# Optimization experiments

Measured on AMD Instinct MI355X. Metric: run time of the kernel, lower is better.

Reference implementation:

```python
import jax, jax.numpy as jnp
import numpy as np

SOS = 1  # start-of-sequence token id (module references a global SOS)
VOCAB, EMBED, HIDDEN = 32000, 512, 1024

def setup_inputs() -> dict:
    key = jax.random.key(0)
    ks = jax.random.split(key, 8)
    B = 32
    s = lambda k, shape, scale: jax.random.normal(k, shape, dtype=jnp.float32) * scale
    return {
        "init_hidden": s(ks[0], (1, B, HIDDEN), 1.0),
        "encoder_outputs": s(ks[1], (B, 64, HIDDEN), 1.0),
        "tgt_len": 64,
        "embedding": s(ks[2], (VOCAB, EMBED), 1.0),
        "w_ih": s(ks[3], (3 * HIDDEN, EMBED), 0.03),
        "b_ih": s(ks[4], (3 * HIDDEN,), 0.03),
        "w_hh": s(ks[5], (3 * HIDDEN, HIDDEN), 0.03),
        "b_hh": s(ks[6], (3 * HIDDEN,), 0.03),
        "w_out": s(ks[7], (VOCAB, HIDDEN), 0.03),
        "b_out": jnp.zeros((VOCAB,), dtype=jnp.float32),
    }

def reference(init_hidden, encoder_outputs, tgt_len, embedding, w_ih, b_ih, w_hh, b_hh, w_out, b_out):
    B = init_hidden.shape[1]
    h0 = init_hidden[0]                       # [B, H] (num_layers=1)
    tok0 = jnp.full((B,), SOS, dtype=jnp.int32)

    def step(carry, _):
        h, tok = carry
        x = jnp.tanh(embedding[tok])          # [B, E]
        gi = x @ w_ih.T + b_ih                # [B, 3H]
        gh = h @ w_hh.T + b_hh                # [B, 3H]
        i_r, i_z, i_n = jnp.split(gi, 3, axis=-1)
        h_r, h_z, h_n = jnp.split(gh, 3, axis=-1)
        r = jax.nn.sigmoid(i_r + h_r)
        z = jax.nn.sigmoid(i_z + h_z)
        n = jnp.tanh(i_n + r * h_n)
        h_new = (1.0 - z) * n + z * h         # [B, H]
        logp = jax.nn.log_softmax(h_new @ w_out.T + b_out, axis=-1)  # [B, V]
        tok_new = jnp.argmax(logp, axis=-1).astype(jnp.int32)
        return (h_new, tok_new), logp

    (_, _), outputs = jax.lax.scan(step, (h0, tok0), None, length=tgt_len)
    return outputs                            # [T, B, V] log-probs (matches list of squeezed outputs)
```

## Files before the change

### kernel.cpp

```cpp
#include <hip/hip_runtime.h>
#include <math.h>

#define B    32
#define H    1024
#define EMB  512
#define V    32000
#define SOS  1

#define OFF_X   0
#define OFF_HA  16384
#define OFF_HB  49152
#define OFF_P   81920
#define OFF_C   145920
#define OFF_HHI 147968
#define OFF_HLO 164352
#define OFF_WHI 180736
#define OFF_WLO 16564736

#define NEG_INF (-3.0e38f)

typedef float f4v   __attribute__((ext_vector_type(4)));
typedef short short8v __attribute__((ext_vector_type(8)));
typedef float f32x4 __attribute__((ext_vector_type(4)));

#define MF(a,b,c) c = __builtin_amdgcn_mfma_f32_16x16x32_bf16(a, b, c, 0, 0, 0)

__device__ __forceinline__ unsigned short rnb(float x) {
    unsigned u = __float_as_uint(x);
    unsigned r = u + 0x7FFFu + ((u >> 16) & 1u);
    return (unsigned short)(r >> 16);
}
__device__ __forceinline__ float bfh(unsigned short s) {
    return __uint_as_float(((unsigned)s) << 16);
}
__device__ __forceinline__ void sm_merge(float& m, float& l, int& a,
                                         float om, float ol, int oa)
{
    const bool take = (om > m) || (om == m && oa < a);
    const float mn = take ? om : m;
    const int   an = take ? oa : a;
    l = l * expf(m - mn) + ol * expf(om - mn);
    m = mn; a = an;
}

__global__ void k_init(const float* __restrict__ ih, const float* __restrict__ emb,
                       const float* __restrict__ wout, float* __restrict__ ws)
{
    const size_t idx = (size_t)blockIdx.x * blockDim.x + threadIdx.x;
    const size_t stride = (size_t)gridDim.x * blockDim.x;
    for (size_t i = idx; i < EMB * B; i += stride)
        ws[OFF_X + i] = tanhf(emb[(size_t)SOS * EMB + (i >> 5)]);
    for (size_t i = idx; i < H * B; i += stride) {
        int j = (int)(i >> 5), b = (int)(i & 31);
        ws[OFF_HA + j * 32 + b] = ih[(size_t)b * H + j];
    }
    short* Whi = (short*)(ws + OFF_WHI);
    short* Wlo = (short*)(ws + OFF_WLO);
    for (size_t i = idx; i < (size_t)V * H; i += stride) {
        const float x = wout[i];
        const unsigned short hi = rnb(x);
        Whi[i] = (short)hi;
        Wlo[i] = (short)rnb(x - bfh(hi));
    }
}

__global__ __launch_bounds__(1024) void k_gru(
    const float* __restrict__ xG, const float* __restrict__ hold,
    const float* __restrict__ wih, const float* __restrict__ bih,
    const float* __restrict__ whh, const float* __restrict__ bhh,
    float* __restrict__ hnew, short* __restrict__ Hhi, short* __restrict__ Hlo)
{
    const int t   = threadIdx.x;
    const int blk = blockIdx.x;
    __shared__ float sred[4 * 1152];

    const int ks = t >> 7;
    const int pl = t & 127;
    const int p  = blk * 128 + pl;
    const int b  = p & 31;
    const int j  = p >> 5;

    float ar = 0.f, az = 0.f, ain = 0.f, ahn = 0.f;
    const int k0 = ks * 192, k1 = k0 + 192;

    const int xe = (k1 < EMB) ? k1 : EMB;
    for (int k = k0; k < xe; k += 4) {
        const float u0 = xG[(k + 0) * 32 + b];
        const float u1 = xG[(k + 1) * 32 + b];
        const float u2 = xG[(k + 2) * 32 + b];
        const float u3 = xG[(k + 3) * 32 + b];
        const float4 w0 = *(const float4*)&wih[(size_t)(0 * H + j) * EMB + k];
        const float4 w1 = *(const float4*)&wih[(size_t)(1 * H + j) * EMB + k];
        const float4 w2 = *(const float4*)&wih[(size_t)(2 * H + j) * EMB + k];
        ar  = fmaf(w0.x, u0, fmaf(w0.y, u1, fmaf(w0.z, u2, fmaf(w0.w, u3, ar))));
        az  = fmaf(w1.x, u0, fmaf(w1.y, u1, fmaf(w1.z, u2, fmaf(w1.w, u3, az))));
        ain = fmaf(w2.x, u0, fmaf(w2.y, u1, fmaf(w2.z, u2, fmaf(w2.w, u3, ain))));
    }
    const int hs = (k0 > EMB) ? k0 : EMB;
    for (int k = hs; k < k1; k += 4) {
        const int kh = k - EMB;
        const float u0 = hold[(kh + 0) * 32 + b];
        const float u1 = hold[(kh + 1) * 32 + b];
        const float u2 = hold[(kh + 2) * 32 + b];
        const float u3 = hold[(kh + 3) * 32 + b];
        const float4 w0 = *(const float4*)&whh[(size_t)(0 * H + j) * H + kh];
        const float4 w1 = *(const float4*)&whh[(size_t)(1 * H + j) * H + kh];
        const float4 w2 = *(const float4*)&whh[(size_t)(2 * H + j) * H + kh];
        ar  = fmaf(w0.x, u0, fmaf(w0.y, u1, fmaf(w0.z, u2, fmaf(w0.w, u3, ar))));
        az  = fmaf(w1.x, u0, fmaf(w1.y, u1, fmaf(w1.z, u2, fmaf(w1.w, u3, az))));
        ahn = fmaf(w2.x, u0, fmaf(w2.y, u1, fmaf(w2.z, u2, fmaf(w2.w, u3, ahn))));
    }

    sred[0 * 1152 + pl * 9 + ks] = ar;
    sred[1 * 1152 + pl * 9 + ks] = az;
    sred[2 * 1152 + pl * 9 + ks] = ain;
    sred[3 * 1152 + pl * 9 + ks] = ahn;
    __syncthreads();

    if (t < 128) {
        const int pp = blk * 128 + t;
        const int bb = pp & 31, jj = pp >> 5;
        float s0 = 0.f, s1 = 0.f, s2 = 0.f, s3 = 0.f;
#pragma unroll
        for (int q = 0; q < 8; ++q) {
            s0 += sred[0 * 1152 + t * 9 + q];
            s1 += sred[1 * 1152 + t * 9 + q];
            s2 += sred[2 * 1152 + t * 9 + q];
            s3 += sred[3 * 1152 + t * 9 + q];
        }
        float gr  = s0 + bih[jj]         + bhh[jj];
        float gz  = s1 + bih[H + jj]     + bhh[H + jj];
        float gin = s2 + bih[2 * H + jj];
        float ghn = s3 + bhh[2 * H + jj];
        float r = 1.f / (1.f + expf(-gr));
        float z = 1.f / (1.f + expf(-gz));
        float n = tanhf(gin + r * ghn);
        const int hidx = jj * 32 + bb;
        const float hv = (1.f - z) * n + z * hold[hidx];
        hnew[hidx] = hv;
        const unsigned short hi = rnb(hv);
        const unsigned short lo = rnb(hv - bfh(hi));
        const int pidx = (((jj >> 3) * 32) + bb) * 8 + (jj & 7);
        Hhi[pidx] = (short)hi;
        Hlo[pidx] = (short)lo;
    }
}

__global__ __launch_bounds__(512, 4) void k_proj(
    const short* __restrict__ Whi, const short* __restrict__ Wlo,
    const short* __restrict__ Hhi, const short* __restrict__ Hlo,
    const float* __restrict__ bout, float* __restrict__ orow,
    float4* __restrict__ P)
{
    __shared__ float Red[4 * 32 * 33];
    __shared__ float Dt[32 * 68];
    __shared__ float bl[64];
    __shared__ float pm[2][32], pls[2][32];
    __shared__ int   pa[2][32];

    const int t   = threadIdx.x;
    const int blk = blockIdx.x;
    const int r0  = blk * 64;
    const int w   = t >> 6;
    const int mh  = w >> 2;
    const int kq  = w & 3;
    const int l   = t & 63;
    const int lr  = l & 15;
    const int lg  = l >> 4;

    if (t < 64) bl[t] = bout[r0 + t];

    const short* pAh = Whi + (size_t)(r0 + mh * 32 + lr) * H + lg * 8;
    const short* pAl = Wlo + (size_t)(r0 + mh * 32 + lr) * H + lg * 8;
    const short* pBh = Hhi + ((size_t)lg * 32 + lr) * 8;
    const short* pBl = Hlo + ((size_t)lg * 32 + lr) * 8;

    f32x4 acc00 = {0.f, 0.f, 0.f, 0.f};
    f32x4 acc01 = {0.f, 0.f, 0.f, 0.f};
    f32x4 acc10 = {0.f, 0.f, 0.f, 0.f};
    f32x4 acc11 = {0.f, 0.f, 0.f, 0.f};

#pragma unroll 2
    for (int i = 0; i < 8; ++i) {
        const int c = 4 * i + kq;
        const short8v a0h = *(const short8v*)(pAh + c * 32);
        const short8v a0l = *(const short8v*)(pAl + c * 32);
        const short8v a1h = *(const short8v*)(pAh + 16 * H + c * 32);
        const short8v a1l = *(const short8v*)(pAl + 16 * H + c * 32);
        const short8v b0h = *(const short8v*)(pBh + c * 1024);
        const short8v b0l = *(const short8v*)(pBl + c * 1024);
        const short8v b1h = *(const short8v*)(pBh + c * 1024 + 128);
        const short8v b1l = *(const short8v*)(pBl + c * 1024 + 128);
        MF(a0h, b0h, acc00); MF(a0h, b0l, acc00); MF(a0l, b0h, acc00);
        MF(a0h, b1h, acc01); MF(a0h, b1l, acc01); MF(a0l, b1h, acc01);
        MF(a1h, b0h, acc10); MF(a1h, b0l, acc10); MF(a1l, b0h, acc10);
        MF(a1h, b1h, acc11); MF(a1h, b1l, acc11); MF(a1l, b1h, acc11);
    }

    if (kq >= 2) {
        float* rp = Red + (mh * 2 + (kq - 2)) * 1056;
#pragma unroll
        for (int mt = 0; mt < 2; ++mt)
#pragma unroll
            for (int r = 0; r < 4; ++r) {
                const int row = mt * 16 + lg * 4 + r;
                rp[row * 33 + lr]      = mt ? acc10[r] : acc00[r];
                rp[row * 33 + 16 + lr] = mt ? acc11[r] : acc01[r];
            }
    }
    __syncthreads();
    if (kq < 2) {
        const float* rp = Red + (mh * 2 + kq) * 1056;
#pragma unroll
        for (int mt = 0; mt < 2; ++mt)
#pragma unroll
            for (int r = 0; r < 4; ++r) {
                const int row = mt * 16 + lg * 4 + r;
                const float e0 = rp[row * 33 + lr];
                const float e1 = rp[row * 33 + 16 + lr];
                if (mt) { acc10[r] += e0; acc11[r] += e1; }
                else    { acc00[r] += e0; acc01[r] += e1; }
            }
    }
    __syncthreads();
    if (kq == 1) {
        float* rp = Red + mh * 2 * 1056;
#pragma unroll
        for (int mt = 0; mt < 2; ++mt)
#pragma unroll
            for (int r = 0; r < 4; ++r) {
                const int row = mt * 16 + lg * 4 + r;
                rp[row * 33 + lr]      = mt ? acc10[r] : acc00[r];
                rp[row * 33 + 16 + lr] = mt ? acc11[r] : acc01[r];
            }
    }
    __syncthreads();

    if (kq == 0) {
        const float* rp = Red + mh * 2 * 1056;
        float val[2][2][4];
#pragma unroll
        for (int mt = 0; mt < 2; ++mt)
#pragma unroll
            for (int r = 0; r < 4; ++r) {
                const int row = mt * 16 + lg * 4 + r;
                const float bo = bl[mh * 32 + row];
                val[mt][0][r] = (mt ? acc10[r] : acc00[r]) + rp[row * 33 + lr] + bo;
                val[mt][1][r] = (mt ? acc11[r] : acc01[r]) + rp[row * 33 + 16 + lr] + bo;
            }
#pragma unroll
        for (int mt = 0; mt < 2; ++mt)
#pragma unroll
            for (int nt = 0; nt < 2; ++nt)
#pragma unroll
                for (int r = 0; r < 4; ++r)
                    Dt[(nt * 16 + lr) * 68 + mh * 32 + mt * 16 + lg * 4 + r] = val[mt][nt][r];

#pragma unroll
        for (int nt = 0; nt < 2; ++nt) {
            float m = val[0][nt][0], ls = 1.f;
            int a = r0 + mh * 32 + lg * 4;
#pragma unroll
            for (int q = 1; q < 8; ++q) {
                const int mt = q >> 2, r = q & 3;
                const float x = val[mt][nt][r];
                const int row = r0 + mh * 32 + mt * 16 + lg * 4 + r;
                if (x > m) { ls = ls * expf(m - x) + 1.f; m = x; a = row; }
                else       { ls += expf(x - m); }
            }
            sm_merge(m, ls, a, __shfl_xor(m, 16), __shfl_xor(ls, 16), __shfl_xor(a, 16));
            sm_merge(m, ls, a, __shfl_xor(m, 32), __shfl_xor(ls, 32), __shfl_xor(a, 32));
            if (lg == 0) { pm[mh][nt * 16 + lr] = m; pls[mh][nt * 16 + lr] = ls; pa[mh][nt * 16 + lr] = a; }
        }
    }
    __syncthreads();

    if (t < 32) {
        float m = pm[0][t], ls = pls[0][t]; int a = pa[0][t];
        sm_merge(m, ls, a, pm[1][t], pls[1][t], pa[1][t]);
        P[blk * 32 + t] = make_float4(m, ls, (float)a, 0.f);
    }

    const int sb = t >> 4, rq = t & 15;
    const f4v v = *(const f4v*)&Dt[sb * 68 + rq * 4];
    __builtin_nontemporal_store(v, (f4v*)&orow[(size_t)sb * V + r0 + rq * 4]);
}

__global__ __launch_bounds__(256) void k_fin2(
    const float4* __restrict__ partial, const float* __restrict__ emb,
    float* __restrict__ xG, float* __restrict__ C)
{
    const int b = blockIdx.x;
    const int t = threadIdx.x;
    __shared__ float fm[256], fl[256];
    __shared__ int   fa[256], stok;

    float m = NEG_INF, l = 0.f; int a = 0x7FFFFFFF;
    {
        float4 p = partial[t * 32 + b];
        m = p.x; l = p.y; a = (int)p.z;
    }
    if (t + 256 < 500) {
        float4 p = partial[(t + 256) * 32 + b];
        sm_merge(m, l, a, p.x, p.y, (int)p.z);
    }
    fm[t] = m; fl[t] = l; fa[t] = a;
    __syncthreads();
    for (int s = 128; s > 0; s >>= 1) {
        if (t < s) {
            const float om = fm[t + s], ol = fl[t + s];
            const int   oa = fa[t + s];
            float mm = fm[t]; float ll = fl[t]; int aa = fa[t];
            const bool take = (om > mm) || (om == mm && oa < aa);
            const float mn = take ? om : mm;
            const int   an = take ? oa : aa;
            ll = ll * expf(mm - mn) + ol * expf(om - mn);
            fm[t] = mn; fl[t] = ll; fa[t] = an;
        }
        __syncthreads();
    }
    if (t == 0) {
        C[b] = fm[0] + logf(fl[0]);
        stok = fa[0];
    }
    __syncthreads();
    const int TOK = stok;
    for (int k = t; k < EMB; k += 256)
        xG[k * 32 + b] = tanhf(emb[(size_t)TOK * EMB + k]);
}

__global__ __launch_bounds__(256) void k_sub(float* __restrict__ out,
                                             const float* __restrict__ C)
{
    const int r = blockIdx.x;
    const float c = C[r];
    f4v* row = (f4v*)(out + (size_t)r * V);
    for (int v = threadIdx.x; v < V / 4; v += 256) {
        f4v x = __builtin_nontemporal_load(&row[v]);
        x -= c;
        __builtin_nontemporal_store(x, &row[v]);
    }
}

extern "C" void kernel_launch(void* const* d_in, const int* in_sizes, int n_in,
                              void* d_out, int out_size, void* d_ws, size_t ws_size,
                              hipStream_t stream)
{
    const float* p_ih   = (const float*)d_in[0];
    const float* p_emb  = (const float*)d_in[3];
    const float* p_wih  = (const float*)d_in[4];
    const float* p_bih  = (const float*)d_in[5];
    const float* p_whh  = (const float*)d_in[6];
    const float* p_bhh  = (const float*)d_in[7];
    const float* p_wout = (const float*)d_in[8];
    const float* p_bout = (const float*)d_in[9];
    float* out = (float*)d_out;
    float* ws  = (float*)d_ws;
    const int T = out_size / (B * V);

    float*  xG  = ws + OFF_X;
    float*  hA  = ws + OFF_HA;
    float*  hB  = ws + OFF_HB;
    float4* P   = (float4*)(ws + OFF_P);
    float*  C   = ws + OFF_C;
    short*  Hhi = (short*)(ws + OFF_HHI);
    short*  Hlo = (short*)(ws + OFF_HLO);
    short*  Whi = (short*)(ws + OFF_WHI);
    short*  Wlo = (short*)(ws + OFF_WLO);

    k_init<<<2048, 256, 0, stream>>>(p_ih, p_emb, p_wout, ws);

    for (int st = 0; st < T; ++st) {
        float* hold = (st & 1) ? hB : hA;
        float* hnew = (st & 1) ? hA : hB;
        float* orow = out + (size_t)st * B * V;
        k_gru<<<256, 1024, 0, stream>>>(xG, hold, p_wih, p_bih, p_whh, p_bhh,
                                        hnew, Hhi, Hlo);
        k_proj<<<500, 512, 0, stream>>>(Whi, Wlo, Hhi, Hlo, p_bout, orow, P);
        k_fin2<<<B, 256, 0, stream>>>(P, p_emb, xG, C + st * B);
    }
    k_sub<<<T * B, 256, 0, stream>>>(out, C);
}
```

Before: 3.733 ms.

## Interleave GRU weights and switch hidden/input to batch-major layout

```diff
diff --git a/kernel.cpp b/kernel.cpp
--- a/kernel.cpp
+++ b/kernel.cpp
@@ -7,15 +7,16 @@
 #define V    32000
 #define SOS  1
 
-#define OFF_X   0
+#define OFF_XG  0
 #define OFF_HA  16384
 #define OFF_HB  49152
 #define OFF_P   81920
 #define OFF_C   145920
 #define OFF_HHI 147968
 #define OFF_HLO 164352
-#define OFF_WHI 180736
-#define OFF_WLO 16564736
+#define OFF_W3  180736
+#define OFF_WHI 4899328
+#define OFF_WLO 21283328
 
 #define NEG_INF (-3.0e38f)
 
@@ -44,15 +45,38 @@
 }
 
 __global__ void k_init(const float* __restrict__ ih, const float* __restrict__ emb,
-                       const float* __restrict__ wout, float* __restrict__ ws)
+                       const float* __restrict__ wout,
+                       const float* __restrict__ wih, const float* __restrict__ whh,
+                       float* __restrict__ ws)
 {
     const size_t idx = (size_t)blockIdx.x * blockDim.x + threadIdx.x;
     const size_t stride = (size_t)gridDim.x * blockDim.x;
-    for (size_t i = idx; i < EMB * B; i += stride)
-        ws[OFF_X + i] = tanhf(emb[(size_t)SOS * EMB + (i >> 5)]);
+
+    for (size_t i = idx; i < EMB * B; i += stride) {
+        const int k = (int)(i >> 5), b = (int)(i & 31);
+        ws[OFF_XG + b * EMB + k] = tanhf(emb[(size_t)SOS * EMB + k]);
+    }
+    short* Hhi = (short*)(ws + OFF_HHI);
+    short* Hlo = (short*)(ws + OFF_HLO);
     for (size_t i = idx; i < H * B; i += stride) {
-        int j = (int)(i >> 5), b = (int)(i & 31);
-        ws[OFF_HA + j * 32 + b] = ih[(size_t)b * H + j];
+        const int j = (int)(i >> 5), b = (int)(i & 31);
+        const float hv = ih[(size_t)b * H + j];
+        ws[OFF_HA + b * H + j] = hv;
+        const unsigned short hi = rnb(hv);
+        const int pidx = ((j >> 3) * 32 + b) * 8 + (j & 7);
+        Hhi[pidx] = (short)hi;
+        Hlo[pidx] = (short)rnb(hv - bfh(hi));
+    }
+    float* W3 = ws + OFF_W3;
+    for (size_t i = idx; i < (size_t)H * 384 * 12; i += stride) {
+        const int j   = (int)(i / (384 * 12));
+        const int rem = (int)(i % (384 * 12));
+        const int kq  = rem / 12;
+        const int g   = (rem % 12) >> 2;
+        const int e   = rem & 3;
+        const int k   = kq * 4 + e;
+        W3[i] = (k < EMB) ? wih[(size_t)(g * H + j) * EMB + k]
+                          : whh[(size_t)(g * H + j) * H + (k - EMB)];
     }
     short* Whi = (short*)(ws + OFF_WHI);
     short* Wlo = (short*)(ws + OFF_WLO);
@@ -66,8 +90,8 @@
 
 __global__ __launch_bounds__(1024) void k_gru(
     const float* __restrict__ xG, const float* __restrict__ hold,
-    const float* __restrict__ wih, const float* __restrict__ bih,
-    const float* __restrict__ whh, const float* __restrict__ bhh,
+    const float* __restrict__ W3,
+    const float* __restrict__ bih, const float* __restrict__ bhh,
     float* __restrict__ hnew, short* __restrict__ Hhi, short* __restrict__ Hlo)
 {
     const int t   = threadIdx.x;
@@ -84,31 +108,31 @@
     const int k0 = ks * 192, k1 = k0 + 192;
 
     const int xe = (k1 < EMB) ? k1 : EMB;
-    for (int k = k0; k < xe; k += 4) {
-        const float u0 = xG[(k + 0) * 32 + b];
-        const float u1 = xG[(k + 1) * 32 + b];
-        const float u2 = xG[(k + 2) * 32 + b];
-        const float u3 = xG[(k + 3) * 32 + b];
-        const float4 w0 = *(const float4*)&wih[(size_t)(0 * H + j) * EMB + k];
-        const float4 w1 = *(const float4*)&wih[(size_t)(1 * H + j) * EMB + k];
-        const float4 w2 = *(const float4*)&wih[(size_t)(2 * H + j) * EMB + k];
-        ar  = fmaf(w0.x, u0, fmaf(w0.y, u1, fmaf(w0.z, u2, fmaf(w0.w, u3, ar))));
-        az  = fmaf(w1.x, u0, fmaf(w1.y, u1, fmaf(w1.z, u2, fmaf(w1.w, u3, az))));
-        ain = fmaf(w2.x, u0, fmaf(w2.y, u1, fmaf(w2.z, u2, fmaf(w2.w, u3, ain))));
+    {
+        const float* w3 = W3 + ((size_t)j * 384 + (k0 >> 2)) * 12;
+        for (int k = k0; k < xe; k += 4, w3 += 12) {
+            const float4 u  = *(const float4*)&xG[b * EMB + k];
+            const float4 w0 = *(const float4*)&w3[0];
+            const float4 w1 = *(const float4*)&w3[4];
+            const float4 w2 = *(const float4*)&w3[8];
+            ar  = fmaf(w0.x, u.x, fmaf(w0.y, u.y, fmaf(w0.z, u.z, fmaf(w0.w, u.w, ar))));
+            az  = fmaf(w1.x, u.x, fmaf(w1.y, u.y, fmaf(w1.z, u.z, fmaf(w1.w, u.w, az))));
+            ain = fmaf(w2.x, u.x, fmaf(w2.y, u.y, fmaf(w2.z, u.z, fmaf(w2.w, u.w, ain))));
+        }
     }
     const int hs = (k0 > EMB) ? k0 : EMB;
-    for (int k = hs; k < k1; k += 4) {
-        const int kh = k - EMB;
-        const float u0 = hold[(kh + 0) * 32 + b];
-        const float u1 = hold[(kh + 1) * 32 + b];
-        const float u2 = hold[(kh + 2) * 32 + b];
-        const float u3 = hold[(kh + 3) * 32 + b];
-        const float4 w0 = *(const float4*)&whh[(size_t)(0 * H + j) * H + kh];
-        const float4 w1 = *(const float4*)&whh[(size_t)(1 * H + j) * H + kh];
-        const float4 w2 = *(const float4*)&whh[(size_t)(2 * H + j) * H + kh];
-        ar  = fmaf(w0.x, u0, fmaf(w0.y, u1, fmaf(w0.z, u2, fmaf(w0.w, u3, ar))));
-        az  = fmaf(w1.x, u0, fmaf(w1.y, u1, fmaf(w1.z, u2, fmaf(w1.w, u3, az))));
-        ahn = fmaf(w2.x, u0, fmaf(w2.y, u1, fmaf(w2.z, u2, fmaf(w2.w, u3, ahn))));
+    {
+        const float* w3 = W3 + ((size_t)j * 384 + (hs >> 2)) * 12;
+        for (int k = hs; k < k1; k += 4, w3 += 12) {
+            const int kh = k - EMB;
+            const float4 u  = *(const float4*)&hold[b * H + kh];
+            const float4 w0 = *(const float4*)&w3[0];
+            const float4 w1 = *(const float4*)&w3[4];
+            const float4 w2 = *(const float4*)&w3[8];
+            ar  = fmaf(w0.x, u.x, fmaf(w0.y, u.y, fmaf(w0.z, u.z, fmaf(w0.w, u.w, ar))));
+            az  = fmaf(w1.x, u.x, fmaf(w1.y, u.y, fmaf(w1.z, u.z, fmaf(w1.w, u.w, az))));
+            ahn = fmaf(w2.x, u.x, fmaf(w2.y, u.y, fmaf(w2.z, u.z, fmaf(w2.w, u.w, ahn))));
+        }
     }
 
     sred[0 * 1152 + pl * 9 + ks] = ar;
@@ -135,12 +159,12 @@
         float r = 1.f / (1.f + expf(-gr));
         float z = 1.f / (1.f + expf(-gz));
         float n = tanhf(gin + r * ghn);
-        const int hidx = jj * 32 + bb;
-        const float hv = (1.f - z) * n + z * hold[hidx];
-        hnew[hidx] = hv;
+        const float ho = hold[bb * H + jj];
+        const float hv = (1.f - z) * n + z * ho;
+        hnew[bb * H + jj] = hv;
         const unsigned short hi = rnb(hv);
         const unsigned short lo = rnb(hv - bfh(hi));
-        const int pidx = (((jj >> 3) * 32) + bb) * 8 + (jj & 7);
+        const int pidx = ((jj >> 3) * 32 + bb) * 8 + (jj & 7);
         Hhi[pidx] = (short)hi;
         Hlo[pidx] = (short)lo;
     }
@@ -278,7 +302,7 @@
     if (t < 32) {
         float m = pm[0][t], ls = pls[0][t]; int a = pa[0][t];
         sm_merge(m, ls, a, pm[1][t], pls[1][t], pa[1][t]);
-        P[blk * 32 + t] = make_float4(m, ls, (float)a, 0.f);
+        P[(size_t)t * 500 + blk] = make_float4(m, ls, (float)a, 0.f);
     }
 
     const int sb = t >> 4, rq = t & 15;
@@ -287,7 +311,7 @@
 }
 
 __global__ __launch_bounds__(256) void k_fin2(
-    const float4* __restrict__ partial, const float* __restrict__ emb,
+    const float4* __restrict__ P, const float* __restrict__ emb,
     float* __restrict__ xG, float* __restrict__ C)
 {
     const int b = blockIdx.x;
@@ -296,26 +320,21 @@
     __shared__ int   fa[256], stok;
 
     float m = NEG_INF, l = 0.f; int a = 0x7FFFFFFF;
-    {
-        float4 p = partial[t * 32 + b];
+    if (t < 500) {
+        const float4 p = P[(size_t)b * 500 + t];
         m = p.x; l = p.y; a = (int)p.z;
     }
     if (t + 256 < 500) {
-        float4 p = partial[(t + 256) * 32 + b];
+        const float4 p = P[(size_t)b * 500 + t + 256];
         sm_merge(m, l, a, p.x, p.y, (int)p.z);
     }
     fm[t] = m; fl[t] = l; fa[t] = a;
     __syncthreads();
     for (int s = 128; s > 0; s >>= 1) {
         if (t < s) {
-            const float om = fm[t + s], ol = fl[t + s];
-            const int   oa = fa[t + s];
             float mm = fm[t]; float ll = fl[t]; int aa = fa[t];
-            const bool take = (om > mm) || (om == mm && oa < aa);
-            const float mn = take ? om : mm;
-            const int   an = take ? oa : aa;
-            ll = ll * expf(mm - mn) + ol * expf(om - mn);
-            fm[t] = mn; fl[t] = ll; fa[t] = an;
+            sm_merge(mm, ll, aa, fm[t + s], fl[t + s], fa[t + s]);
+            fm[t] = mm; fl[t] = ll; fa[t] = aa;
         }
         __syncthreads();
     }
@@ -326,7 +345,7 @@
     __syncthreads();
     const int TOK = stok;
     for (int k = t; k < EMB; k += 256)
-        xG[k * 32 + b] = tanhf(emb[(size_t)TOK * EMB + k]);
+        xG[b * EMB + k] = tanhf(emb[(size_t)TOK * EMB + k]);
 }
 
 __global__ __launch_bounds__(256) void k_sub(float* __restrict__ out,
@@ -358,23 +377,24 @@
     float* ws  = (float*)d_ws;
     const int T = out_size / (B * V);
 
-    float*  xG  = ws + OFF_X;
+    float*  xG  = ws + OFF_XG;
     float*  hA  = ws + OFF_HA;
     float*  hB  = ws + OFF_HB;
     float4* P   = (float4*)(ws + OFF_P);
     float*  C   = ws + OFF_C;
     short*  Hhi = (short*)(ws + OFF_HHI);
     short*  Hlo = (short*)(ws + OFF_HLO);
+    float*  W3  = ws + OFF_W3;
     short*  Whi = (short*)(ws + OFF_WHI);
     short*  Wlo = (short*)(ws + OFF_WLO);
 
-    k_init<<<2048, 256, 0, stream>>>(p_ih, p_emb, p_wout, ws);
+    k_init<<<2048, 256, 0, stream>>>(p_ih, p_emb, p_wout, p_wih, p_whh, ws);
 
     for (int st = 0; st < T; ++st) {
         float* hold = (st & 1) ? hB : hA;
         float* hnew = (st & 1) ? hA : hB;
         float* orow = out + (size_t)st * B * V;
-        k_gru<<<256, 1024, 0, stream>>>(xG, hold, p_wih, p_bih, p_whh, p_bhh,
+        k_gru<<<256, 1024, 0, stream>>>(xG, hold, W3, p_bih, p_bhh,
                                         hnew, Hhi, Hlo);
         k_proj<<<500, 512, 0, stream>>>(Whi, Wlo, Hhi, Hlo, p_bout, orow, P);
         k_fin2<<<B, 256, 0, stream>>>(P, p_emb, xG, C + st * B);
```

New measurement: 4.734 ms. 26.8% more time.

## Fuse argmax/logsumexp finalize and embedding lookup into GRU kernel

Applied to the files above, without the earlier changes.

```diff
diff --git a/kernel.cpp b/kernel.cpp
--- a/kernel.cpp
+++ b/kernel.cpp
@@ -7,7 +7,6 @@
 #define V    32000
 #define SOS  1
 
-#define OFF_X   0
 #define OFF_HA  16384
 #define OFF_HB  49152
 #define OFF_P   81920
@@ -16,12 +15,14 @@
 #define OFF_HLO 164352
 #define OFF_WHI 180736
 #define OFF_WLO 16564736
+#define OFF_PK  32948736
 
 #define NEG_INF (-3.0e38f)
 
 typedef float f4v   __attribute__((ext_vector_type(4)));
 typedef short short8v __attribute__((ext_vector_type(8)));
 typedef float f32x4 __attribute__((ext_vector_type(4)));
+typedef unsigned long long u64;
 
 #define MF(a,b,c) c = __builtin_amdgcn_mfma_f32_16x16x32_bf16(a, b, c, 0, 0, 0)
 
@@ -42,17 +43,28 @@
     l = l * expf(m - mn) + ol * expf(om - mn);
     m = mn; a = an;
 }
-
-__global__ void k_init(const float* __restrict__ ih, const float* __restrict__ emb,
-                       const float* __restrict__ wout, float* __restrict__ ws)
+__device__ __forceinline__ void sm2(float& m, float& l, float om, float ol)
+{
+    const float mn = fmaxf(m, om);
+    l = l * expf(m - mn) + ol * expf(om - mn);
+    m = mn;
+}
+
+__global__ void k_init(const float* __restrict__ ih, const float* __restrict__ wout,
+                       float* __restrict__ ws)
 {
     const size_t idx = (size_t)blockIdx.x * blockDim.x + threadIdx.x;
     const size_t stride = (size_t)gridDim.x * blockDim.x;
-    for (size_t i = idx; i < EMB * B; i += stride)
-        ws[OFF_X + i] = tanhf(emb[(size_t)SOS * EMB + (i >> 5)]);
+    short* Hhi = (short*)(ws + OFF_HHI);
+    short* Hlo = (short*)(ws + OFF_HLO);
     for (size_t i = idx; i < H * B; i += stride) {
         int j = (int)(i >> 5), b = (int)(i & 31);
-        ws[OFF_HA + j * 32 + b] = ih[(size_t)b * H + j];
+        const float hv = ih[(size_t)b * H + j];
+        ws[OFF_HA + j * 32 + b] = hv;
+        const unsigned short hi = rnb(hv);
+        const int pidx = ((j >> 3) * 32 + b) * 8 + (j & 7);
+        Hhi[pidx] = (short)hi;
+        Hlo[pidx] = (short)rnb(hv - bfh(hi));
     }
     short* Whi = (short*)(ws + OFF_WHI);
     short* Wlo = (short*)(ws + OFF_WLO);
@@ -64,15 +76,78 @@
     }
 }
 
-__global__ __launch_bounds__(1024) void k_gru(
-    const float* __restrict__ xG, const float* __restrict__ hold,
+#define XLF   16896
+#define DSMA  ((XLF + 4608 + 2112 + 32) * 4)
+
+__global__ __launch_bounds__(1024) void k_gruf(
+    const float4* __restrict__ P, const u64* __restrict__ Pkey,
+    const float* __restrict__ emb, const float* __restrict__ hold,
     const float* __restrict__ wih, const float* __restrict__ bih,
     const float* __restrict__ whh, const float* __restrict__ bhh,
-    float* __restrict__ hnew, short* __restrict__ Hhi, short* __restrict__ Hlo)
-{
+    float* __restrict__ hnew, short* __restrict__ Hhi, short* __restrict__ Hlo,
+    float* __restrict__ C_prev, int first)
+{
+    extern __shared__ __align__(16) float dsm[];
+    float* xl   = dsm;
+    float* sred = dsm + XLF;
+    u64*   kred = (u64*)(dsm + XLF + 4608);
+    int*   tokl = (int*)(dsm + XLF + 4608 + 2112);
+
     const int t   = threadIdx.x;
     const int blk = blockIdx.x;
-    __shared__ float sred[4 * 1152];
+
+    {
+        const int b = t & 31, seg = t >> 5;
+        float* cm = sred;
+        float* cl = sred + 1056;
+        u64 kk = 0; float m = NEG_INF, lsum = 0.f;
+        if (!first) {
+            for (int e = seg; e < 500; e += 32) {
+                const u64 ke = Pkey[e * 32 + b];
+                if (ke > kk) kk = ke;
+                if (blk == 0) {
+                    const float4 p = P[e * 32 + b];
+                    sm2(m, lsum, p.x, p.y);
+                }
+            }
+        }
+        kred[seg * 33 + b] = kk;
+        if (blk == 0) { cm[seg * 33 + b] = m; cl[seg * 33 + b] = lsum; }
+        __syncthreads();
+        for (int s = 16; s > 0; s >>= 1) {
+            if (t < s * 32) {
+                const u64 o = kred[(seg + s) * 33 + b];
+                if (o > kred[seg * 33 + b]) kred[seg * 33 + b] = o;
+                if (blk == 0) {
+                    float mm = cm[seg * 33 + b], ll = cl[seg * 33 + b];
+                    sm2(mm, ll, cm[(seg + s) * 33 + b], cl[(seg + s) * 33 + b]);
+                    cm[seg * 33 + b] = mm; cl[seg * 33 + b] = ll;
+                }
+            }
+            __syncthreads();
+        }
+        if (t < 32) {
+            tokl[t] = first ? SOS : (int)(~(unsigned)(kred[t] & 0xFFFFFFFFull));
+            if (blk == 0 && !first) C_prev[t] = cm[t] + logf(cl[t]);
+        }
+        __syncthreads();
+    }
+
+    {
+        const int b = t & 31;
+        const int TOK = tokl[b];
+        const int kq0 = t >> 5;
+#pragma unroll
+        for (int it = 0; it < 4; ++it) {
+            const int kq = kq0 + 32 * it;
+            const float4 e4 = *(const float4*)&emb[(size_t)TOK * EMB + kq * 4];
+            xl[(4 * kq + 0) * 33 + b] = tanhf(e4.x);
+            xl[(4 * kq + 1) * 33 + b] = tanhf(e4.y);
+            xl[(4 * kq + 2) * 33 + b] = tanhf(e4.z);
+            xl[(4 * kq + 3) * 33 + b] = tanhf(e4.w);
+        }
+    }
+    __syncthreads();
 
     const int ks = t >> 7;
     const int pl = t & 127;
@@ -85,10 +160,10 @@
 
     const int xe = (k1 < EMB) ? k1 : EMB;
     for (int k = k0; k < xe; k += 4) {
-        const float u0 = xG[(k + 0) * 32 + b];
-        const float u1 = xG[(k + 1) * 32 + b];
-        const float u2 = xG[(k + 2) * 32 + b];
-        const float u3 = xG[(k + 3) * 32 + b];
+        const float u0 = xl[(k + 0) * 33 + b];
+        const float u1 = xl[(k + 1) * 33 + b];
+        const float u2 = xl[(k + 2) * 33 + b];
+        const float u3 = xl[(k + 3) * 33 + b];
         const float4 w0 = *(const float4*)&wih[(size_t)(0 * H + j) * EMB + k];
         const float4 w1 = *(const float4*)&wih[(size_t)(1 * H + j) * EMB + k];
         const float4 w2 = *(const float4*)&wih[(size_t)(2 * H + j) * EMB + k];
@@ -140,7 +215,7 @@
         hnew[hidx] = hv;
         const unsigned short hi = rnb(hv);
         const unsigned short lo = rnb(hv - bfh(hi));
-        const int pidx = (((jj >> 3) * 32) + bb) * 8 + (jj & 7);
+        const int pidx = ((jj >> 3) * 32 + bb) * 8 + (jj & 7);
         Hhi[pidx] = (short)hi;
         Hlo[pidx] = (short)lo;
     }
@@ -150,7 +225,7 @@
     const short* __restrict__ Whi, const short* __restrict__ Wlo,
     const short* __restrict__ Hhi, const short* __restrict__ Hlo,
     const float* __restrict__ bout, float* __restrict__ orow,
-    float4* __restrict__ P)
+    float4* __restrict__ P, u64* __restrict__ Pkey)
 {
     __shared__ float Red[4 * 32 * 33];
     __shared__ float Dt[32 * 68];
@@ -279,6 +354,9 @@
         float m = pm[0][t], ls = pls[0][t]; int a = pa[0][t];
         sm_merge(m, ls, a, pm[1][t], pls[1][t], pa[1][t]);
         P[blk * 32 + t] = make_float4(m, ls, (float)a, 0.f);
+        unsigned u = __float_as_uint(m);
+        u = (u >> 31) ? ~u : (u | 0x80000000u);
+        Pkey[blk * 32 + t] = ((u64)u << 32) | (unsigned)(~(unsigned)a);
     }
 
     const int sb = t >> 4, rq = t & 15;
@@ -286,47 +364,28 @@
     __builtin_nontemporal_store(v, (f4v*)&orow[(size_t)sb * V + r0 + rq * 4]);
 }
 
-__global__ __launch_bounds__(256) void k_fin2(
-    const float4* __restrict__ partial, const float* __restrict__ emb,
-    float* __restrict__ xG, float* __restrict__ C)
-{
-    const int b = blockIdx.x;
+__global__ __launch_bounds__(1024) void k_finlast(
+    const float4* __restrict__ P, float* __restrict__ C_last)
+{
+    __shared__ float fm[1056], fl[1056];
     const int t = threadIdx.x;
-    __shared__ float fm[256], fl[256];
-    __shared__ int   fa[256], stok;
-
-    float m = NEG_INF, l = 0.f; int a = 0x7FFFFFFF;
-    {
-        float4 p = partial[t * 32 + b];
-        m = p.x; l = p.y; a = (int)p.z;
-    }
-    if (t + 256 < 500) {
-        float4 p = partial[(t + 256) * 32 + b];
-        sm_merge(m, l, a, p.x, p.y, (int)p.z);
-    }
-    fm[t] = m; fl[t] = l; fa[t] = a;
-    __syncthreads();
-    for (int s = 128; s > 0; s >>= 1) {
-        if (t < s) {
-            const float om = fm[t + s], ol = fl[t + s];
-            const int   oa = fa[t + s];
-            float mm = fm[t]; float ll = fl[t]; int aa = fa[t];
-            const bool take = (om > mm) || (om == mm && oa < aa);
-            const float mn = take ? om : mm;
-            const int   an = take ? oa : aa;
-            ll = ll * expf(mm - mn) + ol * expf(om - mn);
-            fm[t] = mn; fl[t] = ll; fa[t] = an;
+    const int seg = t >> 5, b = t & 31;
+    float m = NEG_INF, l = 0.f;
+    for (int e = seg; e < 500; e += 32) {
+        const float4 p = P[e * 32 + b];
+        sm2(m, l, p.x, p.y);
+    }
+    fm[seg * 33 + b] = m; fl[seg * 33 + b] = l;
+    __syncthreads();
+    for (int s = 16; s > 0; s >>= 1) {
+        if (t < s * 32) {
+            float mm = fm[seg * 33 + b], ll = fl[seg * 33 + b];
+            sm2(mm, ll, fm[(seg + s) * 33 + b], fl[(seg + s) * 33 + b]);
+            fm[seg * 33 + b] = mm; fl[seg * 33 + b] = ll;
         }
         __syncthreads();
     }
-    if (t == 0) {
-        C[b] = fm[0] + logf(fl[0]);
-        stok = fa[0];
-    }
-    __syncthreads();
-    const int TOK = stok;
-    for (int k = t; k < EMB; k += 256)
-        xG[k * 32 + b] = tanhf(emb[(size_t)TOK * EMB + k]);
+    if (t < 32) C_last[t] = fm[t] + logf(fl[t]);
 }
 
 __global__ __launch_bounds__(256) void k_sub(float* __restrict__ out,
@@ -358,7 +417,6 @@
     float* ws  = (float*)d_ws;
     const int T = out_size / (B * V);
 
-    float*  xG  = ws + OFF_X;
     float*  hA  = ws + OFF_HA;
     float*  hB  = ws + OFF_HB;
     float4* P   = (float4*)(ws + OFF_P);
@@ -367,17 +425,23 @@
     short*  Hlo = (short*)(ws + OFF_HLO);
     short*  Whi = (short*)(ws + OFF_WHI);
     short*  Wlo = (short*)(ws + OFF_WLO);
-
-    k_init<<<2048, 256, 0, stream>>>(p_ih, p_emb, p_wout, ws);
+    u64*    PK  = (u64*)(ws + OFF_PK);
+
+    hipFuncSetAttribute((const void*)k_gruf,
+                        hipFuncAttributeMaxDynamicSharedMemorySize, DSMA);
+
+    k_init<<<2048, 256, 0, stream>>>(p_ih, p_wout, ws);
 
     for (int st = 0; st < T; ++st) {
         float* hold = (st & 1) ? hB : hA;
         float* hnew = (st & 1) ? hA : hB;
         float* orow = out + (size_t)st * B * V;
-        k_gru<<<256, 1024, 0, stream>>>(xG, hold, p_wih, p_bih, p_whh, p_bhh,
-                                        hnew, Hhi, Hlo);
-        k_proj<<<500, 512, 0, stream>>>(Whi, Wlo, Hhi, Hlo, p_bout, orow, P);
-        k_fin2<<<B, 256, 0, stream>>>(P, p_emb, xG, C + st * B);
-    }
+        float* Cprv = C + (st > 0 ? (st - 1) * B : 0);
+        k_gruf<<<256, 1024, DSMA, stream>>>(P, PK, p_emb, hold,
+                                            p_wih, p_bih, p_whh, p_bhh,
+                                            hnew, Hhi, Hlo, Cprv, st == 0 ? 1 : 0);
+        k_proj<<<500, 512, 0, stream>>>(Whi, Wlo, Hhi, Hlo, p_bout, orow, P, PK);
+    }
+    k_finlast<<<1, 1024, 0, stream>>>(P, C + (T - 1) * B);
     k_sub<<<T * B, 256, 0, stream>>>(out, C);
 }
```

Measured after the change: 3.966 ms. 1.06x slower.
